# Kernel tuning notes

Hardware: AMD Instinct MI355X
Metric: run time of the kernel (lower is better)

## Reference

```python
import jax, jax.numpy as jnp
import numpy as np


def setup_inputs() -> dict:
    key = jax.random.key(0)
    ks = jax.random.split(key, 9)
    B = 1024
    s = 0.05
    return {
        "x": jax.random.normal(ks[0], (B, 1024), dtype=jnp.float32),
        "u1": jax.random.normal(ks[1], (8, 8, 16), dtype=jnp.float32) * s,
        "u2": jax.random.normal(ks[2], (8, 8, 16), dtype=jnp.float32) * s,
        "u3": jax.random.normal(ks[3], (16, 16, 16), dtype=jnp.float32) * s,
        "b2": jax.random.normal(ks[4], (16, 16, 16), dtype=jnp.float32) * s,
        "b1_core": jax.random.normal(ks[5], (16, 16), dtype=jnp.float32) * s,
        "bias1": jax.random.normal(ks[6], (8, 8, 16), dtype=jnp.float32) * s,
        "fc2_w": jax.random.normal(ks[7], (10, 1024), dtype=jnp.float32) * s,
        "fc2_b": jax.random.normal(ks[8], (10,), dtype=jnp.float32) * s,
    }


def reference(x, u1, u2, u3, b2, b1_core, bias1, fc2_w, fc2_b):
    batch = x.shape[0]
    t = x.reshape(batch, 8, 8, 16)                       # z a b c
    t = jnp.einsum('zabc,ade->zbcde', t, u1)             # (z,8,16,8,16)
    t = jnp.einsum('zabcd,def->zabcef', t, b2)           # (z,8,16,8,16,16)
    t = jnp.einsum('zabcde,afd->zbcef', t, u2)           # (z,16,8,16,8)
    t = jnp.einsum('zabcd,ce->zabde', t, b1_core)        # (z,16,8,8,16)
    t = jnp.einsum('zabcd,aed->zbce', t, u3)             # (z,8,8,16)
    t = t + bias1
    h = jax.nn.relu(t.reshape(batch, 1024))
    return h @ fc2_w.T + fc2_b
```

## Files before the change

kernel.cpp:

```cpp
#include <hip/hip_runtime.h>


using s16x8 = __attribute__((ext_vector_type(8))) short;
using f32x4 = __attribute__((ext_vector_type(4))) float;

__device__ inline short f2bf(float f) {
    unsigned u = __builtin_bit_cast(unsigned, f);
    u += 0x7fffu + ((u >> 16) & 1u);
    return (short)(u >> 16);
}

__global__ __launch_bounds__(256) void k_prep(
    const float* __restrict__ x, const float* __restrict__ u1,
    const float* __restrict__ u2, const float* __restrict__ u3,
    const float* __restrict__ b2, const float* __restrict__ b1c,
    const float* __restrict__ fc2b, short* __restrict__ Wb,
    short* __restrict__ Xb, float* __restrict__ out) {
    const int blk = blockIdx.x;
    const int tid = threadIdx.x;

    if (blk >= 256) {
        const int base = (blk - 256) * 4096 + tid * 16;
#pragma unroll
        for (int h = 0; h < 2; ++h) {
            float4 f0 = *(const float4*)&x[base + h * 8];
            float4 f1 = *(const float4*)&x[base + h * 8 + 4];
            s16x8 v;
            v[0] = f2bf(f0.x); v[1] = f2bf(f0.y);
            v[2] = f2bf(f0.z); v[3] = f2bf(f0.w);
            v[4] = f2bf(f1.x); v[5] = f2bf(f1.y);
            v[6] = f2bf(f1.z); v[7] = f2bf(f1.w);
            *(s16x8*)&Xb[base + h * 8] = v;
        }
        return;
    }

    __shared__ float C2f[4096];
    __shared__ float T1s[2048];
    __shared__ float T2s[64 * 17];
    const int d = blk >> 5;
    const int r = (blk >> 2) & 7;
    const int t0 = (blk & 3) * 4;

    if (tid < 40) {
        int idx = blk * 40 + tid;
        out[idx] = fc2b[idx % 10];
    }
#pragma unroll
    for (int j = 0; j < 16; ++j) {
        int idx = tid + 256 * j;
        int p = (idx >> 4) & 15, s = idx & 15;
        float acc = 0.f;
#pragma unroll
        for (int q = 0; q < 16; ++q)
            acc += b2[j * 256 + p * 16 + q] * b1c[q * 16 + s];
        C2f[idx] = acc;
    }
    __syncthreads();
#pragma unroll
    for (int j = 0; j < 8; ++j) {
        float acc = 0.f;
#pragma unroll
        for (int e = 0; e < 16; ++e)
            acc += u1[(j * 8 + d) * 16 + e] * C2f[e * 256 + tid];
        T1s[j * 256 + tid] = acc;
    }
    __syncthreads();
#pragma unroll
    for (int j = 0; j < 4; ++j) {
        int idx = tid + 256 * j;
        int ab = idx >> 4, s = idx & 15;
        int a = ab >> 3, b = ab & 7;
        float acc = 0.f;
#pragma unroll
        for (int p = 0; p < 16; ++p)
            acc += T1s[a * 256 + p * 16 + s] * u2[(b * 8 + r) * 16 + p];
        T2s[ab * 17 + s] = acc;
    }
    __syncthreads();
    {
        const int j = tid >> 6;
        const int t = t0 + j;
        const int col0 = (tid & 63) * 16;
        const int ab = col0 >> 4;
        const float* t2p = &T2s[ab * 17];
        short* wrow = &Wb[(blk * 4 + j) * 1024 + col0];
        s16x8 v0, v1;
#pragma unroll
        for (int c = 0; c < 16; ++c) {
            const float* u3p = &u3[c * 256 + t * 16];
            float acc = 0.f;
#pragma unroll
            for (int s = 0; s < 16; ++s) acc += t2p[s] * u3p[s];
            short bf = f2bf(acc);
            if (c < 8) v0[c] = bf; else v1[c - 8] = bf;
        }
        *(s16x8*)(wrow) = v0;
        *(s16x8*)(wrow + 8) = v1;
    }
}

#define LDK 264

__global__ __launch_bounds__(256) void k_gemm(
    const short* __restrict__ Xb, const short* __restrict__ Wb,
    const float* __restrict__ bias, const float* __restrict__ W2,
    float* __restrict__ out) {
    __shared__ short As[64][LDK];
    __shared__ short Bs[64][LDK];
    __shared__ float W2s[10][64];
    const int tid = threadIdx.x;
    const int lane = tid & 63;
    const int w = tid >> 6, wr = w >> 1, wc = w & 1;
    const int z0 = blockIdx.y * 64, o0 = blockIdx.x * 64;
    const int srow = tid >> 2;
    const int sc = (tid & 3) * 16;

    if (tid < 160) {
        int jj = (tid * 4) >> 6, c = (tid * 4) & 63;
        *(float4*)&W2s[jj][c] = *(const float4*)&W2[jj * 1024 + o0 + c];
    }

    const short* xp = &Xb[(z0 + srow) * 1024 + sc];
    const short* wp = &Wb[(o0 + srow) * 1024 + sc];

    f32x4 acc[2][2] = {};
    s16x8 ax[8], bx[8];

#pragma unroll
    for (int h = 0; h < 4; ++h)
#pragma unroll
        for (int q = 0; q < 2; ++q) {
            ax[h * 2 + q] = *(const s16x8*)(xp + h * 64 + q * 8);
            bx[h * 2 + q] = *(const s16x8*)(wp + h * 64 + q * 8);
        }

    for (int k0 = 0; k0 < 1024; k0 += 256) {
#pragma unroll
        for (int h = 0; h < 4; ++h)
#pragma unroll
            for (int q = 0; q < 2; ++q) {
                *(s16x8*)&As[srow][sc + h * 64 + q * 8] = ax[h * 2 + q];
                *(s16x8*)&Bs[srow][sc + h * 64 + q * 8] = bx[h * 2 + q];
            }
        __syncthreads();
        if (k0 + 256 < 1024) {
            const short* xi = xp + k0 + 256;
            const short* wi = wp + k0 + 256;
#pragma unroll
            for (int h = 0; h < 4; ++h)
#pragma unroll
                for (int q = 0; q < 2; ++q) {
                    ax[h * 2 + q] = *(const s16x8*)(xi + h * 64 + q * 8);
                    bx[h * 2 + q] = *(const s16x8*)(wi + h * 64 + q * 8);
                }
        }
#pragma unroll
        for (int ks = 0; ks < 8; ++ks) {
            const int kb = ks * 32 + (lane >> 4) * 8;
            s16x8 a0 = *(const s16x8*)&As[wr * 32 + (lane & 15)][kb];
            s16x8 a1 = *(const s16x8*)&As[wr * 32 + 16 + (lane & 15)][kb];
            s16x8 b0 = *(const s16x8*)&Bs[wc * 32 + (lane & 15)][kb];
            s16x8 b1 = *(const s16x8*)&Bs[wc * 32 + 16 + (lane & 15)][kb];
            acc[0][0] = __builtin_amdgcn_mfma_f32_16x16x32_bf16(a0, b0, acc[0][0], 0, 0, 0);
            acc[0][1] = __builtin_amdgcn_mfma_f32_16x16x32_bf16(a0, b1, acc[0][1], 0, 0, 0);
            acc[1][0] = __builtin_amdgcn_mfma_f32_16x16x32_bf16(a1, b0, acc[1][0], 0, 0, 0);
            acc[1][1] = __builtin_amdgcn_mfma_f32_16x16x32_bf16(a1, b1, acc[1][1], 0, 0, 0);
        }
        __syncthreads();
    }

    float* Ht = (float*)As;
#pragma unroll
    for (int m = 0; m < 2; ++m)
#pragma unroll
        for (int n = 0; n < 2; ++n) {
            const int row = wr * 32 + m * 16 + (lane >> 4) * 4;
            const int col = wc * 32 + n * 16 + (lane & 15);
            const float bv = bias[o0 + col];
#pragma unroll
            for (int j = 0; j < 4; ++j)
                Ht[(row + j) * 132 + col] = fmaxf(acc[m][n][j] + bv, 0.f);
        }
    __syncthreads();

    const int rrow = tid >> 2, q = tid & 3;
    float part[10];
#pragma unroll
    for (int jj = 0; jj < 10; ++jj) part[jj] = 0.f;
#pragma unroll
    for (int cc = 0; cc < 16; ++cc) {
        const int c = q + 4 * cc;
        const float hv = Ht[rrow * 132 + c];
#pragma unroll
        for (int jj = 0; jj < 10; ++jj) part[jj] += hv * W2s[jj][c];
    }
#pragma unroll
    for (int jj = 0; jj < 10; ++jj) {
        float p = part[jj];
        p += __shfl_xor(p, 1);
        p += __shfl_xor(p, 2);
        if (q == 0) atomicAdd(&out[(z0 + rrow) * 10 + jj], p);
    }
}

extern "C" void kernel_launch(void* const* d_in, const int* in_sizes, int n_in,
                              void* d_out, int out_size, void* d_ws, size_t ws_size,
                              hipStream_t stream) {
    const float* x     = (const float*)d_in[0];
    const float* u1    = (const float*)d_in[1];
    const float* u2    = (const float*)d_in[2];
    const float* u3    = (const float*)d_in[3];
    const float* b2    = (const float*)d_in[4];
    const float* b1c   = (const float*)d_in[5];
    const float* bias1 = (const float*)d_in[6];
    const float* fc2w  = (const float*)d_in[7];
    const float* fc2b  = (const float*)d_in[8];
    float* out = (float*)d_out;

    short* Wb = (short*)d_ws;
    short* Xb = (short*)((char*)d_ws + 2u * 1024u * 1024u);

    k_prep<<<512, 256, 0, stream>>>(x, u1, u2, u3, b2, b1c, fc2b, Wb, Xb, out);
    k_gemm<<<dim3(16, 16), 256, 0, stream>>>(Xb, Wb, bias1, fc2w, out);
}
```

Measured before the change: 31.62 us.

## Split GEMM K dimension four ways and reduce partials in a separate output kernel

The 1024x1024x1024 bf16 GEMM now uses a 4-way split-K grid (16x16x4 blocks), so 1024 blocks run instead of 256 and more of the CUs are occupied. Each block writes fp32 partial sums to a 16 MB workspace. A new third kernel sums the four partials, applies bias and ReLU, and computes the 10-wide fc2 projection with full-row wave reductions, which removes the atomics and the out initialisation. In exchange it adds a kernel launch and a large round trip of partial results through global memory.

```diff
diff --git a/kernel.cpp b/kernel.cpp
--- a/kernel.cpp
+++ b/kernel.cpp
@@ -14,8 +14,7 @@
     const float* __restrict__ x, const float* __restrict__ u1,
     const float* __restrict__ u2, const float* __restrict__ u3,
     const float* __restrict__ b2, const float* __restrict__ b1c,
-    const float* __restrict__ fc2b, short* __restrict__ Wb,
-    short* __restrict__ Xb, float* __restrict__ out) {
+    short* __restrict__ Wb, short* __restrict__ Xb) {
     const int blk = blockIdx.x;
     const int tid = threadIdx.x;
 
@@ -42,10 +41,6 @@
     const int r = (blk >> 2) & 7;
     const int t0 = (blk & 3) * 4;
 
-    if (tid < 40) {
-        int idx = blk * 40 + tid;
-        out[idx] = fc2b[idx % 10];
-    }
 #pragma unroll
     for (int j = 0; j < 16; ++j) {
         int idx = tid + 256 * j;
@@ -100,63 +95,55 @@
     }
 }
 
-#define LDK 264
+#define LDK 136
 
 __global__ __launch_bounds__(256) void k_gemm(
     const short* __restrict__ Xb, const short* __restrict__ Wb,
-    const float* __restrict__ bias, const float* __restrict__ W2,
-    float* __restrict__ out) {
+    float* __restrict__ PH) {
     __shared__ short As[64][LDK];
     __shared__ short Bs[64][LDK];
-    __shared__ float W2s[10][64];
     const int tid = threadIdx.x;
     const int lane = tid & 63;
     const int w = tid >> 6, wr = w >> 1, wc = w & 1;
-    const int z0 = blockIdx.y * 64, o0 = blockIdx.x * 64;
+    const int o0 = blockIdx.x * 64, z0 = blockIdx.y * 64, kz = blockIdx.z;
     const int srow = tid >> 2;
     const int sc = (tid & 3) * 16;
 
-    if (tid < 160) {
-        int jj = (tid * 4) >> 6, c = (tid * 4) & 63;
-        *(float4*)&W2s[jj][c] = *(const float4*)&W2[jj * 1024 + o0 + c];
-    }
-
-    const short* xp = &Xb[(z0 + srow) * 1024 + sc];
-    const short* wp = &Wb[(o0 + srow) * 1024 + sc];
+    const short* xp = &Xb[(z0 + srow) * 1024 + kz * 256 + sc];
+    const short* wp = &Wb[(o0 + srow) * 1024 + kz * 256 + sc];
 
     f32x4 acc[2][2] = {};
-    s16x8 ax[8], bx[8];
-
-#pragma unroll
-    for (int h = 0; h < 4; ++h)
+    s16x8 ax[4], bx[4];
+
+#pragma unroll
+    for (int h = 0; h < 2; ++h)
 #pragma unroll
         for (int q = 0; q < 2; ++q) {
             ax[h * 2 + q] = *(const s16x8*)(xp + h * 64 + q * 8);
             bx[h * 2 + q] = *(const s16x8*)(wp + h * 64 + q * 8);
         }
 
-    for (int k0 = 0; k0 < 1024; k0 += 256) {
-#pragma unroll
-        for (int h = 0; h < 4; ++h)
+#pragma unroll
+    for (int it = 0; it < 2; ++it) {
+#pragma unroll
+        for (int h = 0; h < 2; ++h)
 #pragma unroll
             for (int q = 0; q < 2; ++q) {
                 *(s16x8*)&As[srow][sc + h * 64 + q * 8] = ax[h * 2 + q];
                 *(s16x8*)&Bs[srow][sc + h * 64 + q * 8] = bx[h * 2 + q];
             }
         __syncthreads();
-        if (k0 + 256 < 1024) {
-            const short* xi = xp + k0 + 256;
-            const short* wi = wp + k0 + 256;
-#pragma unroll
-            for (int h = 0; h < 4; ++h)
+        if (it == 0) {
+#pragma unroll
+            for (int h = 0; h < 2; ++h)
 #pragma unroll
                 for (int q = 0; q < 2; ++q) {
-                    ax[h * 2 + q] = *(const s16x8*)(xi + h * 64 + q * 8);
-                    bx[h * 2 + q] = *(const s16x8*)(wi + h * 64 + q * 8);
+                    ax[h * 2 + q] = *(const s16x8*)(xp + 128 + h * 64 + q * 8);
+                    bx[h * 2 + q] = *(const s16x8*)(wp + 128 + h * 64 + q * 8);
                 }
         }
 #pragma unroll
-        for (int ks = 0; ks < 8; ++ks) {
+        for (int ks = 0; ks < 4; ++ks) {
             const int kb = ks * 32 + (lane >> 4) * 8;
             s16x8 a0 = *(const s16x8*)&As[wr * 32 + (lane & 15)][kb];
             s16x8 a1 = *(const s16x8*)&As[wr * 32 + 16 + (lane & 15)][kb];
@@ -170,37 +157,54 @@
         __syncthreads();
     }
 
-    float* Ht = (float*)As;
+    float* ph = &PH[(unsigned)kz * 1048576u];
 #pragma unroll
     for (int m = 0; m < 2; ++m)
 #pragma unroll
         for (int n = 0; n < 2; ++n) {
-            const int row = wr * 32 + m * 16 + (lane >> 4) * 4;
-            const int col = wc * 32 + n * 16 + (lane & 15);
-            const float bv = bias[o0 + col];
+            const int row = z0 + wr * 32 + m * 16 + (lane >> 4) * 4;
+            const int col = o0 + wc * 32 + n * 16 + (lane & 15);
 #pragma unroll
             for (int j = 0; j < 4; ++j)
-                Ht[(row + j) * 132 + col] = fmaxf(acc[m][n][j] + bv, 0.f);
-        }
-    __syncthreads();
-
-    const int rrow = tid >> 2, q = tid & 3;
+                ph[(row + j) * 1024 + col] = acc[m][n][j];
+        }
+}
+
+__global__ __launch_bounds__(256) void k_out(
+    const float* __restrict__ PH, const float* __restrict__ bias1,
+    const float* __restrict__ W2, const float* __restrict__ fc2b,
+    float* __restrict__ out) {
+    __shared__ float W2s[10][1024];
+    const int tid = threadIdx.x;
+#pragma unroll
+    for (int i = 0; i < 10; ++i) {
+        const int idx = tid + 256 * i;
+        ((float4*)W2s)[idx] = ((const float4*)W2)[idx];
+    }
+    __syncthreads();
+
+    const int wid = tid >> 6, lane = tid & 63;
+    const int z = blockIdx.x * 4 + wid;
     float part[10];
 #pragma unroll
-    for (int jj = 0; jj < 10; ++jj) part[jj] = 0.f;
-#pragma unroll
-    for (int cc = 0; cc < 16; ++cc) {
-        const int c = q + 4 * cc;
-        const float hv = Ht[rrow * 132 + c];
-#pragma unroll
-        for (int jj = 0; jj < 10; ++jj) part[jj] += hv * W2s[jj][c];
-    }
-#pragma unroll
-    for (int jj = 0; jj < 10; ++jj) {
-        float p = part[jj];
-        p += __shfl_xor(p, 1);
-        p += __shfl_xor(p, 2);
-        if (q == 0) atomicAdd(&out[(z0 + rrow) * 10 + jj], p);
+    for (int j = 0; j < 10; ++j) part[j] = 0.f;
+#pragma unroll
+    for (int i = 0; i < 16; ++i) {
+        const int col = lane + 64 * i;
+        float h = PH[z * 1024 + col] + PH[1048576 + z * 1024 + col]
+                + PH[2097152 + z * 1024 + col] + PH[3145728 + z * 1024 + col];
+        h = fmaxf(h + bias1[col], 0.f);
+#pragma unroll
+        for (int j = 0; j < 10; ++j) part[j] += h * W2s[j][col];
+    }
+#pragma unroll
+    for (int j = 0; j < 10; ++j) {
+#pragma unroll
+        for (int off = 32; off > 0; off >>= 1) part[j] += __shfl_xor(part[j], off);
+    }
+    if (lane == 0) {
+#pragma unroll
+        for (int j = 0; j < 10; ++j) out[z * 10 + j] = part[j] + fc2b[j];
     }
 }
 
@@ -220,7 +224,9 @@
 
     short* Wb = (short*)d_ws;
     short* Xb = (short*)((char*)d_ws + 2u * 1024u * 1024u);
-
-    k_prep<<<512, 256, 0, stream>>>(x, u1, u2, u3, b2, b1c, fc2b, Wb, Xb, out);
-    k_gemm<<<dim3(16, 16), 256, 0, stream>>>(Xb, Wb, bias1, fc2w, out);
-}
+    float* PH = (float*)((char*)d_ws + 4u * 1024u * 1024u);
+
+    k_prep<<<512, 256, 0, stream>>>(x, u1, u2, u3, b2, b1c, Wb, Xb);
+    k_gemm<<<dim3(16, 16, 4), 256, 0, stream>>>(Xb, Wb, PH);
+    k_out<<<256, 256, 0, stream>>>(PH, bias1, fc2w, fc2b, out);
+}
```

Result: no change. 31.78 us (+0.5%).
